# Kernel optimization log

Hardware: AMD Instinct MI355X
Metric: run time of the kernel (lower is better)

## Reference

```python
import jax, jax.numpy as jnp
import numpy as np

B, T, D, H = 2, 2048, 1024, 16
DH = D // H


def setup_inputs() -> dict:
    key = jax.random.key(0)
    ks = jax.random.split(key, 11)
    s = 1.0 / np.sqrt(D)
    return {
        "q": jax.random.normal(ks[0], (B, T, D), jnp.float32),
        "k": jax.random.normal(ks[1], (B, T, D), jnp.float32),
        "v": jax.random.normal(ks[2], (B, T, D), jnp.float32),
        "wq_w": jax.random.normal(ks[3], (D, D), jnp.float32) * s,
        "wq_b": jnp.zeros((D,), jnp.float32),
        "wk_w": jax.random.normal(ks[4], (D, D), jnp.float32) * s,
        "wk_b": jnp.zeros((D,), jnp.float32),
        "wv_w": jax.random.normal(ks[5], (D, D), jnp.float32) * s,
        "wv_b": jnp.zeros((D,), jnp.float32),
        "wo_w": jax.random.normal(ks[6], (D, D), jnp.float32) * s,
        "wo_b": jnp.zeros((D,), jnp.float32),
    }


def reference(q, k, v, wq_w, wq_b, wk_w, wk_b, wv_w, wv_b, wo_w, wo_b):
    b, t, d = q.shape
    # Linear projections (torch Linear: x @ W^T + b)
    wq = (q @ wq_w.T + wq_b).reshape(b, t, H, DH)
    wk = (k @ wk_w.T + wk_b).reshape(b, t, H, DH)
    wv = (v @ wv_w.T + wv_b).reshape(b, t, H, DH)
    # scaled dot-product attention: [b,h,t,s]
    scores = jnp.einsum('bthd,bshd->bhts', wq, wk) / jnp.sqrt(jnp.float32(DH))
    probs = jax.nn.softmax(scores, axis=-1)
    attn = jnp.einsum('bhts,bshd->bthd', probs, wv)  # [b,t,h,dh]
    attn = attn.reshape(b, t, d)
    return attn @ wo_w.T + wo_b
```

## Files before the change

kernel.cpp:

```cpp
#include <hip/hip_runtime.h>
#include <hip/hip_bf16.h>
#include <stdint.h>

#define Bn  2
#define Tn  2048
#define Dn  1024
#define Hn  16
#define DHn 64
#define Mn  (Bn*Tn)

typedef __attribute__((ext_vector_type(8))) short short8;
typedef __attribute__((ext_vector_type(4))) short short4v;
typedef __attribute__((ext_vector_type(4))) float f32x4;

__device__ __forceinline__ f32x4 fzero4() { f32x4 z = {0.f, 0.f, 0.f, 0.f}; return z; }

#define TR16(dst, a32) asm volatile("ds_read_b64_tr_b16 %0, %1" : "=v"(dst) : "v"(a32))

__global__ void cvt3_kernel(const float* __restrict__ a0, const float* __restrict__ a1,
                            const float* __restrict__ a2,
                            __hip_bfloat16* __restrict__ o0, __hip_bfloat16* __restrict__ o1,
                            __hip_bfloat16* __restrict__ o2, int n)
{
    const int i = (blockIdx.x * blockDim.x + threadIdx.x) * 8;
    if (i >= n) return;
    const float* in = blockIdx.y == 0 ? a0 : (blockIdx.y == 1 ? a1 : a2);
    __hip_bfloat16* out = blockIdx.y == 0 ? o0 : (blockIdx.y == 1 ? o1 : o2);
    float4 a = *(const float4*)(in + i);
    float4 b = *(const float4*)(in + i + 4);
    union { __hip_bfloat16 h[8]; short8 u; } tmp;
    tmp.h[0] = __float2bfloat16(a.x); tmp.h[1] = __float2bfloat16(a.y);
    tmp.h[2] = __float2bfloat16(a.z); tmp.h[3] = __float2bfloat16(a.w);
    tmp.h[4] = __float2bfloat16(b.x); tmp.h[5] = __float2bfloat16(b.y);
    tmp.h[6] = __float2bfloat16(b.z); tmp.h[7] = __float2bfloat16(b.w);
    *(short8*)(out + i) = tmp.u;
}

__global__ void cvt4_kernel(const float* __restrict__ a0, const float* __restrict__ a1,
                            const float* __restrict__ a2, const float* __restrict__ a3,
                            __hip_bfloat16* __restrict__ o0, __hip_bfloat16* __restrict__ o1,
                            __hip_bfloat16* __restrict__ o2, __hip_bfloat16* __restrict__ o3, int n)
{
    const int i = (blockIdx.x * blockDim.x + threadIdx.x) * 8;
    if (i >= n) return;
    const float* in = blockIdx.y == 0 ? a0 : (blockIdx.y == 1 ? a1 : (blockIdx.y == 2 ? a2 : a3));
    __hip_bfloat16* out = blockIdx.y == 0 ? o0 : (blockIdx.y == 1 ? o1 : (blockIdx.y == 2 ? o2 : o3));
    float4 a = *(const float4*)(in + i);
    float4 b = *(const float4*)(in + i + 4);
    union { __hip_bfloat16 h[8]; short8 u; } tmp;
    tmp.h[0] = __float2bfloat16(a.x); tmp.h[1] = __float2bfloat16(a.y);
    tmp.h[2] = __float2bfloat16(a.z); tmp.h[3] = __float2bfloat16(a.w);
    tmp.h[4] = __float2bfloat16(b.x); tmp.h[5] = __float2bfloat16(b.y);
    tmp.h[6] = __float2bfloat16(b.z); tmp.h[7] = __float2bfloat16(b.w);
    *(short8*)(out + i) = tmp.u;
}

__global__ __launch_bounds__(256, 2)
void gemm_qkv_kernel(const __hip_bfloat16* __restrict__ qa, const __hip_bfloat16* __restrict__ ka,
                     const __hip_bfloat16* __restrict__ va,
                     const __hip_bfloat16* __restrict__ wq, const __hip_bfloat16* __restrict__ wk,
                     const __hip_bfloat16* __restrict__ wv,
                     const float* __restrict__ bq_, const float* __restrict__ bk_,
                     const float* __restrict__ bv_,
                     __hip_bfloat16* __restrict__ Qp, __hip_bfloat16* __restrict__ Kp,
                     __hip_bfloat16* __restrict__ Vp)
{
    __shared__ alignas(16) short As[2][128*32];
    __shared__ alignas(16) short Bs[2][128*32];
    const int grp = blockIdx.y >> 3;
    const __hip_bfloat16* A  = grp == 0 ? qa : (grp == 1 ? ka : va);
    const __hip_bfloat16* Bw = grp == 0 ? wq : (grp == 1 ? wk : wv);
    const float* bias        = grp == 0 ? bq_ : (grp == 1 ? bk_ : bv_);
    __hip_bfloat16* C        = grp == 0 ? Qp : (grp == 1 ? Kp : Vp);

    const int t = threadIdx.x, lane = t & 63, wave = t >> 6;
    const int wm = wave >> 1, wn = wave & 1;
    const int row0 = blockIdx.x * 128, col0 = (blockIdx.y & 7) * 128;

    f32x4 acc[4][4];
#pragma unroll
    for (int m = 0; m < 4; ++m)
#pragma unroll
        for (int n = 0; n < 4; ++n) acc[m][n] = fzero4();

    const int srow = wave*16 + (lane >> 2);
    const int skk  = (lane & 3) * 8;
    const int ldsb = wave * 1024;

    auto STAGE = [&](int buf, int k0) {
#pragma unroll
        for (int i = 0; i < 2; ++i) {
            __builtin_amdgcn_global_load_lds(
                (const __attribute__((address_space(1))) void*)(A + (size_t)(row0 + i*64 + srow)*Dn + k0 + skk),
                (__attribute__((address_space(3))) void*)((char*)As[buf] + i*4096 + ldsb), 16, 0, 0);
            __builtin_amdgcn_global_load_lds(
                (const __attribute__((address_space(1))) void*)(Bw + (size_t)(col0 + i*64 + srow)*Dn + k0 + skk),
                (__attribute__((address_space(3))) void*)((char*)Bs[buf] + i*4096 + ldsb), 16, 0, 0);
        }
    };

    STAGE(0, 0);
    __syncthreads();
    int cur = 0;
    for (int k0 = 0; k0 < Dn; k0 += 32) {
        if (k0 + 32 < Dn) STAGE(cur ^ 1, k0 + 32);
        short8 af[4], bf_[4];
#pragma unroll
        for (int m = 0; m < 4; ++m)
            af[m] = *(const short8*)((char*)As[cur] + (wm*64 + m*16 + (lane & 15))*64 + (lane >> 4)*16);
#pragma unroll
        for (int n = 0; n < 4; ++n)
            bf_[n] = *(const short8*)((char*)Bs[cur] + (wn*64 + n*16 + (lane & 15))*64 + (lane >> 4)*16);
        __builtin_amdgcn_s_setprio(1);
#pragma unroll
        for (int m = 0; m < 4; ++m)
#pragma unroll
            for (int n = 0; n < 4; ++n)
                acc[m][n] = __builtin_amdgcn_mfma_f32_16x16x32_bf16(af[m], bf_[n], acc[m][n], 0, 0, 0);
        __builtin_amdgcn_s_setprio(0);
        __syncthreads();
        cur ^= 1;
    }

#pragma unroll
    for (int n = 0; n < 4; ++n) {
        const int col = col0 + wn*64 + n*16 + (lane & 15);
        const float bv = bias[col];
#pragma unroll
        for (int m = 0; m < 4; ++m) {
            const int rb_ = row0 + wm*64 + m*16 + (lane>>4)*4;
#pragma unroll
            for (int i = 0; i < 4; ++i)
                C[(size_t)(rb_+i)*Dn + col] = __float2bfloat16(acc[m][n][i] + bv);
        }
    }
}

__global__ __launch_bounds__(256, 2)
void gemm_out_kernel(const __hip_bfloat16* __restrict__ A,
                     const __hip_bfloat16* __restrict__ Bw,
                     const float* __restrict__ bias,
                     float* __restrict__ C)
{
    __shared__ alignas(16) short As[2][64*32];
    __shared__ alignas(16) short Bs[2][128*32];
    const int t = threadIdx.x, lane = t & 63, wave = t >> 6;
    const int wm = wave >> 1, wn = wave & 1;
    const int row0 = blockIdx.x * 64, col0 = blockIdx.y * 128;

    f32x4 acc[2][4];
#pragma unroll
    for (int m = 0; m < 2; ++m)
#pragma unroll
        for (int n = 0; n < 4; ++n) acc[m][n] = fzero4();

    const int srow = wave*16 + (lane >> 2);
    const int skk  = (lane & 3) * 8;
    const int ldsb = wave * 1024;

    auto STAGE = [&](int buf, int k0) {
        __builtin_amdgcn_global_load_lds(
            (const __attribute__((address_space(1))) void*)(A + (size_t)(row0 + srow)*Dn + k0 + skk),
            (__attribute__((address_space(3))) void*)((char*)As[buf] + ldsb), 16, 0, 0);
#pragma unroll
        for (int i = 0; i < 2; ++i)
            __builtin_amdgcn_global_load_lds(
                (const __attribute__((address_space(1))) void*)(Bw + (size_t)(col0 + i*64 + srow)*Dn + k0 + skk),
                (__attribute__((address_space(3))) void*)((char*)Bs[buf] + i*4096 + ldsb), 16, 0, 0);
    };

    STAGE(0, 0);
    __syncthreads();
    int cur = 0;
    for (int k0 = 0; k0 < Dn; k0 += 32) {
        if (k0 + 32 < Dn) STAGE(cur ^ 1, k0 + 32);
        short8 af[2], bf_[4];
#pragma unroll
        for (int m = 0; m < 2; ++m)
            af[m] = *(const short8*)((char*)As[cur] + (wm*32 + m*16 + (lane & 15))*64 + (lane >> 4)*16);
#pragma unroll
        for (int n = 0; n < 4; ++n)
            bf_[n] = *(const short8*)((char*)Bs[cur] + (wn*64 + n*16 + (lane & 15))*64 + (lane >> 4)*16);
        __builtin_amdgcn_s_setprio(1);
#pragma unroll
        for (int m = 0; m < 2; ++m)
#pragma unroll
            for (int n = 0; n < 4; ++n)
                acc[m][n] = __builtin_amdgcn_mfma_f32_16x16x32_bf16(af[m], bf_[n], acc[m][n], 0, 0, 0);
        __builtin_amdgcn_s_setprio(0);
        __syncthreads();
        cur ^= 1;
    }

#pragma unroll
    for (int n = 0; n < 4; ++n) {
        const int col = col0 + wn*64 + n*16 + (lane & 15);
        const float bv = bias[col];
#pragma unroll
        for (int m = 0; m < 2; ++m) {
            const int rb_ = row0 + wm*32 + m*16 + (lane>>4)*4;
#pragma unroll
            for (int i = 0; i < 4; ++i)
                C[(size_t)(rb_+i)*Dn + col] = acc[m][n][i] + bv;
        }
    }
}

#define VPL 1288

__global__ __launch_bounds__(256, 2)
void attn_kernel(const __hip_bfloat16* __restrict__ Q,
                 const __hip_bfloat16* __restrict__ K,
                 const __hip_bfloat16* __restrict__ V,
                 __hip_bfloat16* __restrict__ O)
{
    __shared__ alignas(16) short Vlds[2*2*4*VPL];
    const int t = threadIdx.x, lane = t & 63, wave = t >> 6;
    const int g = lane >> 4, c = lane & 15;
    const int pk = wave & 1, qh = wave >> 1;
    const int blk = (blockIdx.x & 7) * 64 + (blockIdx.x >> 3);
    const int qb = blk & 15;
    const int h  = (blk >> 4) & (Hn - 1);
    const int b  = blk >> 8;
    const size_t base = (size_t)b * Tn * Dn + (size_t)h * DHn;
    const int q0 = qb * 128 + qh * 64;
    const float cexp = 0.18033688011112042f;

    short8 bq[4][2];
#pragma unroll
    for (int qs = 0; qs < 4; ++qs) {
        const __hip_bfloat16* qp = Q + base + (size_t)(q0 + qs*16 + c) * Dn + g*8;
        bq[qs][0] = *(const short8*)qp;
        bq[qs][1] = *(const short8*)(qp + 32);
    }
    short8 ones;
#pragma unroll
    for (int i = 0; i < 8; ++i) ones[i] = (short)0x3F80;

    f32x4 o_[4][4];
#pragma unroll
    for (int qs = 0; qs < 4; ++qs)
#pragma unroll
        for (int d = 0; d < 4; ++d) o_[qs][d] = fzero4();
    float m_[4] = {-3e38f, -3e38f, -3e38f, -3e38f};
    f32x4 lacc[4] = {fzero4(), fzero4(), fzero4(), fzero4()};

    const int vrow = t >> 3;
    const int vd0  = ((t>>1)&3)*VPL + (vrow>>2)*80 + (vrow&3)*16 + (t&1)*8;
    const int vcol = (((t>>1)&3)*16 + (t&1)*8);
    const uint32_t vbase = (uint32_t)(uintptr_t)(void*)Vlds;
    const uint32_t atr = vbase + (uint32_t)(pk*10304 + g*160 + c*8);

    short8 ck[4][2], nk[4][2];
    {
        const __hip_bfloat16* kp = K + base + (size_t)(pk*64 + c) * Dn + g*8;
#pragma unroll
        for (int sub = 0; sub < 4; ++sub)
#pragma unroll
            for (int ks = 0; ks < 2; ++ks)
                ck[sub][ks] = *(const short8*)(kp + (size_t)sub*16*Dn + ks*32);
    }

    for (int it = 0; it < 16; ++it) {
        const int kv0 = it * 128;
        short8 cv[2][2];
#pragma unroll
        for (int p = 0; p < 2; ++p) {
            const __hip_bfloat16* vp = V + base + (size_t)(kv0 + p*64 + vrow) * Dn + vcol;
            cv[p][0] = *(const short8*)vp;
            cv[p][1] = *(const short8*)(vp + (size_t)32*Dn);
        }
        {
            const int kvn = (it < 15) ? kv0 + 128 + pk*64 : pk*64;
            const __hip_bfloat16* kp = K + base + (size_t)(kvn + c) * Dn + g*8;
#pragma unroll
            for (int sub = 0; sub < 4; ++sub)
#pragma unroll
                for (int ks = 0; ks < 2; ++ks)
                    nk[sub][ks] = *(const short8*)(kp + (size_t)sub*16*Dn + ks*32);
        }

        short8 pa[4][2];
#pragma unroll
        for (int qs = 0; qs < 4; ++qs) {
            f32x4 s_[4];
#pragma unroll
            for (int sub = 0; sub < 4; ++sub) s_[sub] = fzero4();
            __builtin_amdgcn_s_setprio(1);
#pragma unroll
            for (int sub = 0; sub < 4; ++sub)
#pragma unroll
                for (int ks = 0; ks < 2; ++ks)
                    s_[sub] = __builtin_amdgcn_mfma_f32_16x16x32_bf16(
                        ck[sub][ks], bq[qs][ks], s_[sub], 0, 0, 0);
            __builtin_amdgcn_s_setprio(0);

            float rm = s_[0][0];
#pragma unroll
            for (int sub = 0; sub < 4; ++sub)
#pragma unroll
                for (int i = 0; i < 4; ++i) rm = fmaxf(rm, s_[sub][i]);
            if (!__all((rm - m_[qs]) * cexp <= 8.0f)) {
                float gm = fmaxf(rm, __shfl_xor(rm, 16));
                gm = fmaxf(gm, __shfl_xor(gm, 32));
                const float mn = fmaxf(m_[qs], gm);
                const float sc = exp2f((m_[qs] - mn) * cexp);
                m_[qs] = mn;
#pragma unroll
                for (int i = 0; i < 4; ++i) lacc[qs][i] *= sc;
#pragma unroll
                for (int d = 0; d < 4; ++d)
#pragma unroll
                    for (int i = 0; i < 4; ++i) o_[qs][d][i] *= sc;
            }
            const float mn = m_[qs];
#pragma unroll
            for (int kc = 0; kc < 2; ++kc)
#pragma unroll
                for (int hf = 0; hf < 2; ++hf)
#pragma unroll
                    for (int i = 0; i < 4; ++i) {
                        const float p = exp2f((s_[kc*2+hf][i] - mn) * cexp);
                        union { __hip_bfloat16 hb; short u; } cvp;
                        cvp.hb = __float2bfloat16(p);
                        pa[qs][kc][hf*4 + i] = cvp.u;
                    }
            lacc[qs] = __builtin_amdgcn_mfma_f32_16x16x32_bf16(ones, pa[qs][0], lacc[qs], 0, 0, 0);
            lacc[qs] = __builtin_amdgcn_mfma_f32_16x16x32_bf16(ones, pa[qs][1], lacc[qs], 0, 0, 0);
        }

        short* vb = Vlds + (it & 1) * 10304;
#pragma unroll
        for (int p = 0; p < 2; ++p) {
            *(short8*)(vb + p*5152 + vd0)       = cv[p][0];
            *(short8*)(vb + p*5152 + vd0 + 640) = cv[p][1];
        }
        asm volatile("s_waitcnt lgkmcnt(0)" ::: "memory");
        __builtin_amdgcn_s_barrier();
        __builtin_amdgcn_sched_barrier(0);

        const uint32_t atrb = atr + (uint32_t)((it & 1) * 20608u);
        short4v tv[4][2][2];
#pragma unroll
        for (int d = 0; d < 4; ++d)
#pragma unroll
            for (int kc = 0; kc < 2; ++kc) {
                const uint32_t a = atrb + (uint32_t)(d*2576 + kc*1280);
                TR16(tv[d][kc][0], a);
                TR16(tv[d][kc][1], a + 640);
            }
#pragma unroll
        for (int d = 0; d < 4; ++d) {
            if (d == 0)      asm volatile("s_waitcnt lgkmcnt(12)" ::: "memory");
            else if (d == 1) asm volatile("s_waitcnt lgkmcnt(8)" ::: "memory");
            else if (d == 2) asm volatile("s_waitcnt lgkmcnt(4)" ::: "memory");
            else             asm volatile("s_waitcnt lgkmcnt(0)" ::: "memory");
            __builtin_amdgcn_sched_barrier(0);
            const short8 av0 = __builtin_shufflevector(tv[d][0][0], tv[d][0][1], 0,1,2,3,4,5,6,7);
            const short8 av1 = __builtin_shufflevector(tv[d][1][0], tv[d][1][1], 0,1,2,3,4,5,6,7);
            __builtin_amdgcn_s_setprio(1);
#pragma unroll
            for (int qs = 0; qs < 4; ++qs) {
                o_[qs][d] = __builtin_amdgcn_mfma_f32_16x16x32_bf16(av0, pa[qs][0], o_[qs][d], 0, 0, 0);
                o_[qs][d] = __builtin_amdgcn_mfma_f32_16x16x32_bf16(av1, pa[qs][1], o_[qs][d], 0, 0, 0);
            }
            __builtin_amdgcn_s_setprio(0);
        }
#pragma unroll
        for (int sub = 0; sub < 4; ++sub)
#pragma unroll
            for (int ks = 0; ks < 2; ++ks) ck[sub][ks] = nk[sub][ks];
    }

    __syncthreads();
    float* cbase = (float*)Vlds;
    if (pk == 1) {
        float* cb = cbase + qh * 4608;
#pragma unroll
        for (int qs = 0; qs < 4; ++qs)
#pragma unroll
            for (int d = 0; d < 4; ++d)
                *(f32x4*)(cb + ((qs*4 + d)*64 + lane)*4) = o_[qs][d];
#pragma unroll
        for (int qs = 0; qs < 4; ++qs) {
            cb[4096 + qs*64 + lane] = m_[qs];
            cb[4352 + qs*64 + lane] = lacc[qs][0];
        }
    }
    __syncthreads();
    if (pk == 0) {
        float* cb = cbase + qh * 4608;
#pragma unroll
        for (int qs = 0; qs < 4; ++qs) {
            const float m1 = cb[4096 + qs*64 + lane];
            const float l1 = cb[4352 + qs*64 + lane];
            const float mN = fmaxf(m_[qs], m1);
            const float sc0 = exp2f((m_[qs] - mN) * cexp);
            const float sc1 = exp2f((m1 - mN) * cexp);
            const float inv = 1.f / (lacc[qs][0]*sc0 + l1*sc1);
            __hip_bfloat16* op = O + base + (size_t)(q0 + qs*16 + c) * Dn + g*4;
#pragma unroll
            for (int d = 0; d < 4; ++d) {
                const f32x4 o1 = *(const f32x4*)(cb + ((qs*4 + d)*64 + lane)*4);
                union { __hip_bfloat16 hb[4]; ushort4 u4; } w;
#pragma unroll
                for (int i = 0; i < 4; ++i)
                    w.hb[i] = __float2bfloat16((o_[qs][d][i]*sc0 + o1[i]*sc1) * inv);
                *(ushort4*)(op + d*16) = w.u4;
            }
        }
    }
}

extern "C" void kernel_launch(void* const* d_in, const int* in_sizes, int n_in,
                              void* d_out, int out_size, void* d_ws, size_t ws_size,
                              hipStream_t stream)
{
    (void)in_sizes; (void)n_in; (void)out_size; (void)ws_size;
    const float* q    = (const float*)d_in[0];
    const float* k    = (const float*)d_in[1];
    const float* v    = (const float*)d_in[2];
    const float* wq_w = (const float*)d_in[3];
    const float* wq_b = (const float*)d_in[4];
    const float* wk_w = (const float*)d_in[5];
    const float* wk_b = (const float*)d_in[6];
    const float* wv_w = (const float*)d_in[7];
    const float* wv_b = (const float*)d_in[8];
    const float* wo_w = (const float*)d_in[9];
    const float* wo_b = (const float*)d_in[10];

    char* ws = (char*)d_ws;
    const size_t S1 = (size_t)Mn * Dn * 2;
    const size_t W  = (size_t)Dn * Dn * 2;
    __hip_bfloat16* qb  = (__hip_bfloat16*)(ws);
    __hip_bfloat16* kb  = (__hip_bfloat16*)(ws + S1);
    __hip_bfloat16* vb  = (__hip_bfloat16*)(ws + 2*S1);
    __hip_bfloat16* wqb = (__hip_bfloat16*)(ws + 3*S1);
    __hip_bfloat16* wkb = (__hip_bfloat16*)(ws + 3*S1 + W);
    __hip_bfloat16* wvb = (__hip_bfloat16*)(ws + 3*S1 + 2*W);
    __hip_bfloat16* wob = (__hip_bfloat16*)(ws + 3*S1 + 3*W);
    __hip_bfloat16* Qp  = (__hip_bfloat16*)(ws + 3*S1 + 4*W);
    __hip_bfloat16* Kp  = (__hip_bfloat16*)(ws + 4*S1 + 4*W);
    __hip_bfloat16* Vp  = (__hip_bfloat16*)(ws + 5*S1 + 4*W);
    __hip_bfloat16* Ap  = (__hip_bfloat16*)(ws + 6*S1 + 4*W);

    const int nQKV = Mn * Dn;
    const int nW   = Dn * Dn;
    cvt3_kernel<<<dim3(nQKV/2048, 3), 256, 0, stream>>>(q, k, v, qb, kb, vb, nQKV);
    cvt4_kernel<<<dim3(nW/2048, 4), 256, 0, stream>>>(wq_w, wk_w, wv_w, wo_w,
                                                      wqb, wkb, wvb, wob, nW);

    gemm_qkv_kernel<<<dim3(Mn/128, 24), 256, 0, stream>>>(
        qb, kb, vb, wqb, wkb, wvb, wq_b, wk_b, wv_b, Qp, Kp, Vp);

    attn_kernel<<<Bn*Hn*(Tn/128), 256, 0, stream>>>(Qp, Kp, Vp, Ap);

    gemm_out_kernel<<<dim3(Mn/64, Dn/128), 256, 0, stream>>>(Ap, wob, wo_b, (float*)d_out);
}
```

Before: 142.6 us.

## Fuse fp32-to-bf16 activation conversion into QKV GEMM and double-buffer attention K registers

Removes the separate activation conversion kernel. The QKV GEMM now loads fp32 q/k/v tiles into registers, converts them to bf16, and writes them to LDS after the MFMA block, so the bf16 activation buffers are never written to or read back from global memory. The attention loop is unrolled by two with ping-pong K register arrays, which drops the per-iteration register copy. The trade-off is that every one of the 8 column blocks now reads A as fp32 (twice the bytes) and the A staging goes through VGPRs instead of direct global-to-LDS loads, which raises register pressure.

```diff
diff --git a/kernel.cpp b/kernel.cpp
--- a/kernel.cpp
+++ b/kernel.cpp
@@ -16,25 +16,6 @@
 __device__ __forceinline__ f32x4 fzero4() { f32x4 z = {0.f, 0.f, 0.f, 0.f}; return z; }
 
 #define TR16(dst, a32) asm volatile("ds_read_b64_tr_b16 %0, %1" : "=v"(dst) : "v"(a32))
-
-__global__ void cvt3_kernel(const float* __restrict__ a0, const float* __restrict__ a1,
-                            const float* __restrict__ a2,
-                            __hip_bfloat16* __restrict__ o0, __hip_bfloat16* __restrict__ o1,
-                            __hip_bfloat16* __restrict__ o2, int n)
-{
-    const int i = (blockIdx.x * blockDim.x + threadIdx.x) * 8;
-    if (i >= n) return;
-    const float* in = blockIdx.y == 0 ? a0 : (blockIdx.y == 1 ? a1 : a2);
-    __hip_bfloat16* out = blockIdx.y == 0 ? o0 : (blockIdx.y == 1 ? o1 : o2);
-    float4 a = *(const float4*)(in + i);
-    float4 b = *(const float4*)(in + i + 4);
-    union { __hip_bfloat16 h[8]; short8 u; } tmp;
-    tmp.h[0] = __float2bfloat16(a.x); tmp.h[1] = __float2bfloat16(a.y);
-    tmp.h[2] = __float2bfloat16(a.z); tmp.h[3] = __float2bfloat16(a.w);
-    tmp.h[4] = __float2bfloat16(b.x); tmp.h[5] = __float2bfloat16(b.y);
-    tmp.h[6] = __float2bfloat16(b.z); tmp.h[7] = __float2bfloat16(b.w);
-    *(short8*)(out + i) = tmp.u;
-}
 
 __global__ void cvt4_kernel(const float* __restrict__ a0, const float* __restrict__ a1,
                             const float* __restrict__ a2, const float* __restrict__ a3,
@@ -56,8 +37,8 @@
 }
 
 __global__ __launch_bounds__(256, 2)
-void gemm_qkv_kernel(const __hip_bfloat16* __restrict__ qa, const __hip_bfloat16* __restrict__ ka,
-                     const __hip_bfloat16* __restrict__ va,
+void gemm_qkv_kernel(const float* __restrict__ qa, const float* __restrict__ ka,
+                     const float* __restrict__ va,
                      const __hip_bfloat16* __restrict__ wq, const __hip_bfloat16* __restrict__ wk,
                      const __hip_bfloat16* __restrict__ wv,
                      const float* __restrict__ bq_, const float* __restrict__ bk_,
@@ -68,7 +49,7 @@
     __shared__ alignas(16) short As[2][128*32];
     __shared__ alignas(16) short Bs[2][128*32];
     const int grp = blockIdx.y >> 3;
-    const __hip_bfloat16* A  = grp == 0 ? qa : (grp == 1 ? ka : va);
+    const float* A           = grp == 0 ? qa : (grp == 1 ? ka : va);
     const __hip_bfloat16* Bw = grp == 0 ? wq : (grp == 1 ? wk : wv);
     const float* bias        = grp == 0 ? bq_ : (grp == 1 ? bk_ : bv_);
     __hip_bfloat16* C        = grp == 0 ? Qp : (grp == 1 ? Kp : Vp);
@@ -85,25 +66,44 @@
 
     const int srow = wave*16 + (lane >> 2);
     const int skk  = (lane & 3) * 8;
-    const int ldsb = wave * 1024;
-
-    auto STAGE = [&](int buf, int k0) {
+    const int ldsb = wave * 1024 + (lane & 63) * 16;
+
+    float4 ra[2][2];
+    auto LOAD_A = [&](int k0) {
 #pragma unroll
         for (int i = 0; i < 2; ++i) {
-            __builtin_amdgcn_global_load_lds(
-                (const __attribute__((address_space(1))) void*)(A + (size_t)(row0 + i*64 + srow)*Dn + k0 + skk),
-                (__attribute__((address_space(3))) void*)((char*)As[buf] + i*4096 + ldsb), 16, 0, 0);
+            const float* ap = A + (size_t)(row0 + i*64 + srow)*Dn + k0 + skk;
+            ra[i][0] = *(const float4*)ap;
+            ra[i][1] = *(const float4*)(ap + 4);
+        }
+    };
+    auto WRITE_A = [&](int buf) {
+#pragma unroll
+        for (int i = 0; i < 2; ++i) {
+            union { __hip_bfloat16 h[8]; short8 u; } w;
+            w.h[0] = __float2bfloat16(ra[i][0].x); w.h[1] = __float2bfloat16(ra[i][0].y);
+            w.h[2] = __float2bfloat16(ra[i][0].z); w.h[3] = __float2bfloat16(ra[i][0].w);
+            w.h[4] = __float2bfloat16(ra[i][1].x); w.h[5] = __float2bfloat16(ra[i][1].y);
+            w.h[6] = __float2bfloat16(ra[i][1].z); w.h[7] = __float2bfloat16(ra[i][1].w);
+            *(short8*)((char*)As[buf] + i*4096 + ldsb) = w.u;
+        }
+    };
+    auto STAGE_B = [&](int buf, int k0) {
+#pragma unroll
+        for (int i = 0; i < 2; ++i)
             __builtin_amdgcn_global_load_lds(
                 (const __attribute__((address_space(1))) void*)(Bw + (size_t)(col0 + i*64 + srow)*Dn + k0 + skk),
-                (__attribute__((address_space(3))) void*)((char*)Bs[buf] + i*4096 + ldsb), 16, 0, 0);
-        }
+                (__attribute__((address_space(3))) void*)((char*)Bs[buf] + i*4096 + wave*1024 + (lane&63)*16), 16, 0, 0);
     };
 
-    STAGE(0, 0);
+    LOAD_A(0);
+    STAGE_B(0, 0);
+    WRITE_A(0);
     __syncthreads();
     int cur = 0;
     for (int k0 = 0; k0 < Dn; k0 += 32) {
-        if (k0 + 32 < Dn) STAGE(cur ^ 1, k0 + 32);
+        const bool more = (k0 + 32 < Dn);
+        if (more) { LOAD_A(k0 + 32); STAGE_B(cur ^ 1, k0 + 32); }
         short8 af[4], bf_[4];
 #pragma unroll
         for (int m = 0; m < 4; ++m)
@@ -118,6 +118,8 @@
             for (int n = 0; n < 4; ++n)
                 acc[m][n] = __builtin_amdgcn_mfma_f32_16x16x32_bf16(af[m], bf_[n], acc[m][n], 0, 0, 0);
         __builtin_amdgcn_s_setprio(0);
+        __builtin_amdgcn_sched_barrier(0);
+        if (more) WRITE_A(cur ^ 1);
         __syncthreads();
         cur ^= 1;
     }
@@ -251,17 +253,17 @@
     const uint32_t vbase = (uint32_t)(uintptr_t)(void*)Vlds;
     const uint32_t atr = vbase + (uint32_t)(pk*10304 + g*160 + c*8);
 
-    short8 ck[4][2], nk[4][2];
+    short8 akA[4][2], akB[4][2];
     {
         const __hip_bfloat16* kp = K + base + (size_t)(pk*64 + c) * Dn + g*8;
 #pragma unroll
         for (int sub = 0; sub < 4; ++sub)
 #pragma unroll
             for (int ks = 0; ks < 2; ++ks)
-                ck[sub][ks] = *(const short8*)(kp + (size_t)sub*16*Dn + ks*32);
-    }
-
-    for (int it = 0; it < 16; ++it) {
+                akA[sub][ks] = *(const short8*)(kp + (size_t)sub*16*Dn + ks*32);
+    }
+
+    auto ITER = [&](const short8 (&ck)[4][2], short8 (&nk)[4][2], int it) {
         const int kv0 = it * 128;
         short8 cv[2][2];
 #pragma unroll
@@ -366,10 +368,11 @@
             }
             __builtin_amdgcn_s_setprio(0);
         }
-#pragma unroll
-        for (int sub = 0; sub < 4; ++sub)
-#pragma unroll
-            for (int ks = 0; ks < 2; ++ks) ck[sub][ks] = nk[sub][ks];
+    };
+
+    for (int j = 0; j < 8; ++j) {
+        ITER(akA, akB, 2*j);
+        ITER(akB, akA, 2*j + 1);
     }
 
     __syncthreads();
@@ -432,26 +435,21 @@
     char* ws = (char*)d_ws;
     const size_t S1 = (size_t)Mn * Dn * 2;
     const size_t W  = (size_t)Dn * Dn * 2;
-    __hip_bfloat16* qb  = (__hip_bfloat16*)(ws);
-    __hip_bfloat16* kb  = (__hip_bfloat16*)(ws + S1);
-    __hip_bfloat16* vb  = (__hip_bfloat16*)(ws + 2*S1);
-    __hip_bfloat16* wqb = (__hip_bfloat16*)(ws + 3*S1);
-    __hip_bfloat16* wkb = (__hip_bfloat16*)(ws + 3*S1 + W);
-    __hip_bfloat16* wvb = (__hip_bfloat16*)(ws + 3*S1 + 2*W);
-    __hip_bfloat16* wob = (__hip_bfloat16*)(ws + 3*S1 + 3*W);
-    __hip_bfloat16* Qp  = (__hip_bfloat16*)(ws + 3*S1 + 4*W);
-    __hip_bfloat16* Kp  = (__hip_bfloat16*)(ws + 4*S1 + 4*W);
-    __hip_bfloat16* Vp  = (__hip_bfloat16*)(ws + 5*S1 + 4*W);
-    __hip_bfloat16* Ap  = (__hip_bfloat16*)(ws + 6*S1 + 4*W);
-
-    const int nQKV = Mn * Dn;
-    const int nW   = Dn * Dn;
-    cvt3_kernel<<<dim3(nQKV/2048, 3), 256, 0, stream>>>(q, k, v, qb, kb, vb, nQKV);
+    __hip_bfloat16* wqb = (__hip_bfloat16*)(ws);
+    __hip_bfloat16* wkb = (__hip_bfloat16*)(ws + W);
+    __hip_bfloat16* wvb = (__hip_bfloat16*)(ws + 2*W);
+    __hip_bfloat16* wob = (__hip_bfloat16*)(ws + 3*W);
+    __hip_bfloat16* Qp  = (__hip_bfloat16*)(ws + 4*W);
+    __hip_bfloat16* Kp  = (__hip_bfloat16*)(ws + 4*W + S1);
+    __hip_bfloat16* Vp  = (__hip_bfloat16*)(ws + 4*W + 2*S1);
+    __hip_bfloat16* Ap  = (__hip_bfloat16*)(ws + 4*W + 3*S1);
+
+    const int nW = Dn * Dn;
     cvt4_kernel<<<dim3(nW/2048, 4), 256, 0, stream>>>(wq_w, wk_w, wv_w, wo_w,
                                                       wqb, wkb, wvb, wob, nW);
 
     gemm_qkv_kernel<<<dim3(Mn/128, 24), 256, 0, stream>>>(
-        qb, kb, vb, wqb, wkb, wvb, wq_b, wk_b, wv_b, Qp, Kp, Vp);
+        q, k, v, wqb, wkb, wvb, wq_b, wk_b, wv_b, Qp, Kp, Vp);
 
     attn_kernel<<<Bn*Hn*(Tn/128), 256, 0, stream>>>(Qp, Kp, Vp, Ap);
 
```

Result: faster. 136.5 us (-4.3%).
